# Performance work log

Measured on AMD Instinct MI355X. Metric: run time of the kernel, lower is better.

Reference implementation:

```python
import jax, jax.numpy as jnp
import numpy as np
from jax import lax


def _ln(x, g, b, eps=1e-5):
    m = jnp.mean(x, axis=-1, keepdims=True)
    v = jnp.mean((x - m) ** 2, axis=-1, keepdims=True)
    return (x - m) / jnp.sqrt(v + eps) * g + b


def _lin(x, w, b):  # torch Linear: w [out,in]
    return x @ w.T + b


def _conv(x, w, b, stride, pad):
    y = lax.conv_general_dilated(x, w, (stride, stride), pad,
                                 dimension_numbers=('NCHW', 'OIHW', 'NCHW'))
    return y + b[None, :, None, None]


def _haar_dwt(x):
    # J=1 haar, zero mode, even H/W: per 2x2 block [[a,b],[c,d]]
    a = x[:, :, 0::2, 0::2]
    bb = x[:, :, 0::2, 1::2]
    c = x[:, :, 1::2, 0::2]
    d = x[:, :, 1::2, 1::2]
    ll = (a + bb + c + d) * 0.5
    lohi = (a - bb + c - d) * 0.5  # band 0 (col-high)
    hilo = (a + bb - c - d) * 0.5  # band 1 (row-high)
    hihi = (a - bb - c + d) * 0.5  # band 2
    return ll, lohi, hilo, hihi


def _cross_attention(q, k, v):
    # q,k,v: [b, d, c]; 8 equal chunks along d; softmax over QUERY axis (torch dim=1)
    b, d, c = q.shape
    chunk = d // 8
    qc = q.reshape(b, 8, chunk, c)
    kc = k.reshape(b, 8, chunk, c)
    vc = v.reshape(b, 8, chunk, c)
    att = jnp.einsum('bnqc,bnkc->bnqk', qc, kc) * (8.0 ** -0.5)
    att = jax.nn.softmax(att, axis=2)  # normalize over q (matches F.softmax dim=1)
    out = jnp.einsum('bnqk,bnkc->bnqc', att, vc)
    return out.reshape(b, d, c)


def _ffn(x, ln1_g, ln1_b, fc1_w, fc1_b, div_w, div_b, fc2_w, fc2_b,
         ln3_g, ln3_b, fc3a_w, fc3a_b, fc3b_w, fc3b_b, lnn_g, lnn_b, act_w, act_b):
    x1 = jax.nn.gelu(_lin(_ln(x, ln1_g, ln1_b), fc1_w, fc1_b), approximate=False)
    x2 = jax.nn.gelu(_lin(x, div_w, div_b), approximate=False) - x1
    x2 = jax.nn.gelu(_lin(x2, fc2_w, fc2_b), approximate=False)
    x3 = _lin(jax.nn.gelu(_lin(_ln(x, ln3_g, ln3_b), fc3a_w, fc3a_b), approximate=False), fc3b_w, fc3b_b)
    gate = jax.nn.sigmoid(_lin(x, act_w, act_b))
    # dropout(0.5) is identity in eval mode
    return gate * _ln(x2 + x3, lnn_g, lnn_b)


def _resize_bilinear_ac(x, oh, ow):
    # bilinear, align_corners=True
    B, C, H, W = x.shape
    def idx(n_in, n_out):
        pos = jnp.linspace(0.0, n_in - 1.0, n_out)
        i0 = jnp.floor(pos).astype(jnp.int32)
        i1 = jnp.minimum(i0 + 1, n_in - 1)
        return i0, i1, (pos - i0).astype(x.dtype)
    y0, y1, wy = idx(H, oh)
    x0, x1, wx = idx(W, ow)
    r = x[:, :, y0, :] * (1 - wy)[None, None, :, None] + x[:, :, y1, :] * wy[None, None, :, None]
    return r[:, :, :, x0] * (1 - wx)[None, None, None, :] + r[:, :, :, x1] * wx[None, None, None, :]


def setup_inputs() -> dict:
    key = jax.random.key(0)
    ks = jax.random.split(key, 25)
    B, Cin, H, W = 16, 128, 128, 128
    Ch = 128  # out_planes // 2
    def nrm(k, shp, s=0.02):
        return jax.random.normal(k, shp, jnp.float32) * s
    inp = {
        'x': jax.random.normal(ks[0], (B, Cin, H, W), jnp.float32),
        'conv1_w': nrm(ks[1], (Ch, 2 * Cin, 1, 1)), 'conv1_b': jnp.zeros((Ch,), jnp.float32),
        'l1_w': nrm(ks[2], (Ch, Cin, 4, 4)), 'l1_b': jnp.zeros((Ch,), jnp.float32),
        'ln1_g': jnp.ones((Ch,), jnp.float32), 'ln1_b': jnp.zeros((Ch,), jnp.float32),
        'fc1_w': nrm(ks[3], (Ch, Ch)), 'fc1_b': jnp.zeros((Ch,), jnp.float32),
        'div_w': nrm(ks[4], (Ch, Ch)), 'div_b': jnp.zeros((Ch,), jnp.float32),
        'fc2_w': nrm(ks[5], (Ch, Ch)), 'fc2_b': jnp.zeros((Ch,), jnp.float32),
        'ln3_g': jnp.ones((Ch,), jnp.float32), 'ln3_b': jnp.zeros((Ch,), jnp.float32),
        'fc3a_w': nrm(ks[6], (Ch, Ch)), 'fc3a_b': jnp.zeros((Ch,), jnp.float32),
        'fc3b_w': nrm(ks[7], (Ch, Ch)), 'fc3b_b': jnp.zeros((Ch,), jnp.float32),
        'lnn_g': jnp.ones((Ch,), jnp.float32), 'lnn_b': jnp.zeros((Ch,), jnp.float32),
        'act_w': nrm(ks[8], (Ch, Ch)), 'act_b': jnp.zeros((Ch,), jnp.float32),
    }
    return inp


def reference(x, conv1_w, conv1_b, l1_w, l1_b, ln1_g, ln1_b, fc1_w, fc1_b,
              div_w, div_b, fc2_w, fc2_b, ln3_g, ln3_b, fc3a_w, fc3a_b,
              fc3b_w, fc3b_b, lnn_g, lnn_b, act_w, act_b):
    dw = jax.nn.relu(_conv(x, l1_w, l1_b, 2, ((1, 1), (1, 1))))
    yL, y_HL, y_LH, y_HH = _haar_dwt(x)
    y = _conv(jnp.concatenate((y_HL, y_LH), axis=1), conv1_w, conv1_b, 1, ((0, 0), (0, 0)))
    b, c, h, w = y.shape
    y_t = y.transpose(0, 2, 3, 1).reshape(b, h * w, c)
    yL_t = yL.transpose(0, 2, 3, 1).reshape(b, h * w, c)
    yHH_t = y_HH.transpose(0, 2, 3, 1).reshape(b, h * w, c)
    att = _cross_attention(yL_t, y_t, yHH_t)
    att = _ffn(att, ln1_g, ln1_b, fc1_w, fc1_b, div_w, div_b, fc2_w, fc2_b,
               ln3_g, ln3_b, fc3a_w, fc3a_b, fc3b_w, fc3b_b, lnn_g, lnn_b, act_w, act_b)
    att = att.reshape(b, h, w, c).transpose(0, 3, 1, 2)
    y_img = y_t.reshape(b, h, w, c).transpose(0, 3, 1, 2)
    down_2x = _resize_bilinear_ac(x, h, w)
    att = att * (down_2x - dw)
    return att + y_img
```

## Files before the change

kernel.cpp:

```cpp
#include <hip/hip_runtime.h>
#include <cmath>


#define EPI_NONE 0
#define EPI_EXP 5

typedef unsigned short u16;
typedef __bf16 v8bf __attribute__((ext_vector_type(8)));
typedef float f32x4 __attribute__((ext_vector_type(4)));

__device__ __forceinline__ float gelu_f(float v) {
  return 0.5f * v * (1.f + erff(v * 0.70710678118654752f));
}
__device__ __forceinline__ float sigmoid_f(float v) {
  return 1.f / (1.f + __expf(-v));
}
__device__ __forceinline__ float bf2f(u16 h) {
  return __uint_as_float((unsigned)h << 16);
}
__device__ __forceinline__ u16 f2bf(float f) {
  unsigned u = __float_as_uint(f);
  return (u16)((u + 0x7fffu + ((u >> 16) & 1u)) >> 16);
}
__device__ __forceinline__ unsigned f2bf_pk(float lo, float hi) {
  unsigned a = __float_as_uint(lo), b = __float_as_uint(hi);
  a = (a + 0x7fffu + ((a >> 16) & 1u)) >> 16;
  b = (b + 0x7fffu + ((b >> 16) & 1u)) >> 16;
  return a | (b << 16);
}
__device__ __forceinline__ void gld_lds16(const void* g, void* l) {
  __builtin_amdgcn_global_load_lds(
      (const __attribute__((address_space(1))) unsigned int*)g,
      (__attribute__((address_space(3))) unsigned int*)l, 16, 0, 0);
}

__global__ __launch_bounds__(256) void pre_k(const float* __restrict__ x,
                                             u16* __restrict__ yL16,
                                             u16* __restrict__ yHHt16,
                                             u16* __restrict__ hllh16,
                                             u16* __restrict__ xpt) {
  int gx = blockIdx.x;
  int jt = gx & 1, cit = gx >> 1;
  int i = blockIdx.y, b = blockIdx.z;
  int j0 = jt * 32, ci0 = cit * 32;
  int tx = threadIdx.x & 31, ty = threadIdx.x >> 5;
  __shared__ float sll[32][33], shl[32][33], slh[32][33], shh[32][33];
  if (gx == 0) {
    int pl = 1 + ((threadIdx.x >> 7) << 1);
    long off = ((long)(b * 4 + pl) * 4160 + (long)i * 65) * 128 + (threadIdx.x & 127);
    xpt[off] = 0;
  } else if (gx == 1) {
    int pl = (threadIdx.x >> 7) << 1;
    long off = ((long)(b * 4 + pl) * 4160 + (long)i * 65 + 64) * 128 + (threadIdx.x & 127);
    xpt[off] = 0;
  }
  const float2* x2 = (const float2*)x;
#pragma unroll
  for (int k = 0; k < 4; ++k) {
    int ci = ty + 8 * k;
    long base = (((long)b * 128 + ci0 + ci) * 128 + 2 * i) * 64 + j0 + tx;
    float2 ab = x2[base];
    float2 cd = x2[base + 64];
    float a = ab.x, bb = ab.y, c = cd.x, d = cd.y;
    sll[ci][tx] = (a + bb + c + d) * 0.5f;
    shl[ci][tx] = (a - bb + c - d) * 0.5f;
    slh[ci][tx] = (a + bb - c - d) * 0.5f;
    shh[ci][tx] = (a - bb - c + d) * 0.5f;
  }
  __syncthreads();
  long tok = (long)b * 4096 + i * 64 + j0;
  int r = threadIdx.x >> 3;
  int q4 = (threadIdx.x & 7) << 2;
  float vll[4], vhl[4], vlh[4], vhh[4];
#pragma unroll
  for (int e = 0; e < 4; ++e) {
    vll[e] = sll[q4 + e][r];
    vhl[e] = shl[q4 + e][r];
    vlh[e] = slh[q4 + e][r];
    vhh[e] = shh[q4 + e][r];
  }
  uint2 u;
  u.x = f2bf_pk(vll[0], vll[1]);
  u.y = f2bf_pk(vll[2], vll[3]);
  *(uint2*)(yL16 + (tok + r) * 128 + ci0 + q4) = u;
  u.x = f2bf_pk(vhl[0], vhl[1]);
  u.y = f2bf_pk(vhl[2], vhl[3]);
  *(uint2*)(hllh16 + (tok + r) * 256 + ci0 + q4) = u;
  u.x = f2bf_pk(vlh[0], vlh[1]);
  u.y = f2bf_pk(vlh[2], vlh[3]);
  *(uint2*)(hllh16 + (tok + r) * 256 + 128 + ci0 + q4) = u;
  {
    int ch = threadIdx.x >> 3;
    int t4 = (threadIdx.x & 7) << 2;
    uint2 h;
    h.x = f2bf_pk(shh[ch][t4], shh[ch][t4 + 1]);
    h.y = f2bf_pk(shh[ch][t4 + 2], shh[ch][t4 + 3]);
    *(uint2*)(yHHt16 + (long)(ci0 + ch) * 65536 + tok + t4) = h;
  }
  {
    long rb = (long)(b * 4) * 4160 + (long)i * 65;
    int ci = j0 + r;
    float pA[4], pB[4], pC[4], pD[4];
#pragma unroll
    for (int e = 0; e < 4; ++e) {
      pA[e] = 0.5f * (vll[e] + vhl[e] + vlh[e] + vhh[e]);
      pB[e] = 0.5f * (vll[e] - vhl[e] + vlh[e] - vhh[e]);
      pC[e] = 0.5f * (vll[e] + vhl[e] - vlh[e] - vhh[e]);
      pD[e] = 0.5f * (vll[e] - vhl[e] - vlh[e] + vhh[e]);
    }
    u.x = f2bf_pk(pA[0], pA[1]);
    u.y = f2bf_pk(pA[2], pA[3]);
    *(uint2*)(xpt + (rb + ci) * 128 + ci0 + q4) = u;
    u.x = f2bf_pk(pB[0], pB[1]);
    u.y = f2bf_pk(pB[2], pB[3]);
    *(uint2*)(xpt + (rb + 4160 + ci + 1) * 128 + ci0 + q4) = u;
    u.x = f2bf_pk(pC[0], pC[1]);
    u.y = f2bf_pk(pC[2], pC[3]);
    *(uint2*)(xpt + (rb + 8320 + ci) * 128 + ci0 + q4) = u;
    u.x = f2bf_pk(pD[0], pD[1]);
    u.y = f2bf_pk(pD[2], pD[3]);
    *(uint2*)(xpt + (rb + 12480 + ci + 1) * 128 + ci0 + q4) = u;
  }
}

__global__ __launch_bounds__(256) void wcvt8_k(
    const float* __restrict__ a0, const float* __restrict__ a1,
    const float* __restrict__ a2, const float* __restrict__ a3,
    const float* __restrict__ a4, const float* __restrict__ a5,
    const float* __restrict__ a6, const float* __restrict__ a7,
    unsigned* __restrict__ dst, unsigned* __restrict__ zp) {
  if (blockIdx.x >= 768) {
    zp[(blockIdx.x - 768) * 256 + threadIdx.x] = 0;
    return;
  }
  int f = blockIdx.x * 256 + threadIdx.x;
  int e = 2 * f;
  if (e < 262144) {
    int ch = e >> 13, kg = (e >> 10) & 7, n = (e >> 3) & 127, ke = e & 7;
    int k = ch * 64 + kg * 8 + ke;
    int stg = ch >> 2, sub = ch & 3;
    int kwsel = sub >> 1, chalf = sub & 1;
    int kh = stg >> 1, cp = stg & 1;
    int kw = cp ? (kwsel ? 2 : 0) : (kwsel ? 3 : 1);
    int c = chalf * 64 + (k & 63);
    long si = (((long)n * 128 + c) * 4 + kh) * 4 + kw;
    dst[f] = f2bf_pk(a0[si], a0[si + 16]);
    return;
  }
  const float* s; int b;
  if (e < 294912)      { s = a1; b = 262144; }
  else if (e < 311296) { s = a2; b = 294912; }
  else if (e < 327680) { s = a3; b = 311296; }
  else if (e < 344064) { s = a4; b = 327680; }
  else if (e < 360448) { s = a5; b = 344064; }
  else if (e < 376832) { s = a6; b = 360448; }
  else                 { s = a7; b = 376832; }
  dst[f] = f2bf_pk(s[e - b], s[e - b + 1]);
}

template <int AMODE, int EPI>
__global__ __launch_bounds__(256) void gemm16_k(
    const u16* __restrict__ A, long sA, int lda,
    const u16* __restrict__ B, long sB, int ldb,
    u16* __restrict__ C, long sC, int ldc,
    int K, float alpha, const float* __restrict__ bias,
    const u16* __restrict__ aux, const float* __restrict__ sc) {
  __shared__ __align__(16) char smem[32768];
  char* As = smem;
  char* Bs = smem + 16384;
  int z = blockIdx.z;
  int tid = threadIdx.x, lane = tid & 63, w = tid >> 6;
  int wm = w >> 1, wn = w & 1, l15 = lane & 15, l4 = lane >> 4;
  const u16* Ab = A + (long)z * sA + (long)blockIdx.x * 128 * lda;
  const u16* Bb = B + (long)z * sB + (long)blockIdx.y * 128 * ldb;
  const float* scz = (AMODE == 1) ? sc + (long)z * K : nullptr;
  int sm = tid >> 3, skg = tid & 7;
  int sbase = sm * 128 + ((skg ^ (sm & 7)) << 4);
  uint4 pa[4], pb[4];

  auto loadAB = [&](int k0) {
#pragma unroll
    for (int u = 0; u < 4; ++u) {
      pb[u] = *(const uint4*)(Bb + (long)(sm + 32 * u) * ldb + k0 + skg * 8);
      uint4 v = *(const uint4*)(Ab + (long)(sm + 32 * u) * lda + k0 + skg * 8);
      if (AMODE == 1) {
        float4 s0 = *(const float4*)(scz + k0 + skg * 8);
        float4 s1 = *(const float4*)(scz + k0 + skg * 8 + 4);
        v.x = f2bf_pk(bf2f((u16)(v.x & 0xffff)) * s0.x, bf2f((u16)(v.x >> 16)) * s0.y);
        v.y = f2bf_pk(bf2f((u16)(v.y & 0xffff)) * s0.z, bf2f((u16)(v.y >> 16)) * s0.w);
        v.z = f2bf_pk(bf2f((u16)(v.z & 0xffff)) * s1.x, bf2f((u16)(v.z >> 16)) * s1.y);
        v.w = f2bf_pk(bf2f((u16)(v.w & 0xffff)) * s1.z, bf2f((u16)(v.w >> 16)) * s1.w);
      }
      pa[u] = v;
    }
  };

  f32x4 acc[4][4] = {};
  loadAB(0);
  int nch = K >> 6;
  for (int ch = 0; ch < nch; ++ch) {
    __syncthreads();
#pragma unroll
    for (int u = 0; u < 4; ++u) {
      *(uint4*)(As + sbase + u * 4096) = pa[u];
      *(uint4*)(Bs + sbase + u * 4096) = pb[u];
    }
    __syncthreads();
    if (ch + 1 < nch) loadAB((ch + 1) << 6);
#pragma unroll
    for (int s = 0; s < 2; ++s) {
      int ko = (((s << 2) | l4) ^ (l15 & 7)) << 4;
      v8bf af[4], bfr[4];
#pragma unroll
      for (int t = 0; t < 4; ++t) {
        af[t] = *(const v8bf*)(As + (64 * wm + 16 * t + l15) * 128 + ko);
        bfr[t] = *(const v8bf*)(Bs + (64 * wn + 16 * t + l15) * 128 + ko);
      }
#pragma unroll
      for (int mt = 0; mt < 4; ++mt)
#pragma unroll
        for (int nt = 0; nt < 4; ++nt)
          acc[mt][nt] = __builtin_amdgcn_mfma_f32_16x16x32_bf16(af[mt], bfr[nt], acc[mt][nt], 0, 0, 0);
    }
  }
  u16* Cb = C + (long)z * sC;
#pragma unroll
  for (int mt = 0; mt < 4; ++mt) {
#pragma unroll
    for (int nt = 0; nt < 4; ++nt) {
      f32x4 a = acc[mt][nt];
      int n = blockIdx.y * 128 + 64 * wn + 16 * nt + l15;
      float bv = bias ? bias[n] : 0.f;
#pragma unroll
      for (int r = 0; r < 4; ++r) {
        long m = (long)blockIdx.x * 128 + 64 * wm + 16 * mt + 4 * l4 + r;
        float v = a[r] * alpha + bv;
        if (EPI == EPI_EXP) v = __expf(v);
        Cb[m * ldc + n] = f2bf(v);
      }
    }
  }
}

__global__ __launch_bounds__(256) void ffn_k(
    const u16* __restrict__ Xg,
    const u16* __restrict__ w_fc1, const u16* __restrict__ w_div,
    const u16* __restrict__ w_fc2, const u16* __restrict__ w_fc3a,
    const u16* __restrict__ w_fc3b, const u16* __restrict__ w_act,
    const float* __restrict__ b_fc1, const float* __restrict__ b_div,
    const float* __restrict__ b_fc2, const float* __restrict__ b_fc3a,
    const float* __restrict__ b_fc3b, const float* __restrict__ b_act,
    const float* __restrict__ ln1g, const float* __restrict__ ln1b,
    const float* __restrict__ ln3g, const float* __restrict__ ln3b,
    const float* __restrict__ lnng, const float* __restrict__ lnnb,
    u16* __restrict__ out) {
  __shared__ __align__(16) char smem[49152];
  char* X = smem;
  char* A = smem + 16384;
  char* E = smem + 32768;
  int z = blockIdx.x;
  long t0 = (long)z * 64;
  int tid = threadIdx.x, lane = tid & 63, w = tid >> 6;
  int wm = w >> 1, wn = w & 1, l15 = lane & 15, l4 = lane >> 4;

  {
    const u16* src = Xg + t0 * 128;
#pragma unroll
    for (int r = 0; r < 4; ++r) {
      int u = r * 256 + tid;
      int row = u >> 4, cg = u & 15;
      gld_lds16(src + row * 128 + ((cg ^ (row & 7)) << 3),
                X + (r * 256 + w * 64) * 16);
    }
  }

  auto gemm = [&](const char* Asrc, const u16* Bg, f32x4 (&acc)[2][4]) {
#pragma unroll
    for (int mt = 0; mt < 2; ++mt)
#pragma unroll
      for (int nt = 0; nt < 4; ++nt) acc[mt][nt] = f32x4{0.f, 0.f, 0.f, 0.f};
#pragma unroll
    for (int s = 0; s < 4; ++s) {
      v8bf af[2], bw[4];
#pragma unroll
      for (int mt = 0; mt < 2; ++mt) {
        int row = 32 * wm + 16 * mt + l15;
        af[mt] = *(const v8bf*)(Asrc + row * 256 + (((s * 4 + l4) ^ (row & 7)) << 4));
      }
#pragma unroll
      for (int nt = 0; nt < 4; ++nt) {
        int rn = 64 * wn + 16 * nt + l15;
        bw[nt] = *(const v8bf*)(Bg + rn * 128 + (s * 4 + l4) * 8);
      }
#pragma unroll
      for (int mt = 0; mt < 2; ++mt)
#pragma unroll
        for (int nt = 0; nt < 4; ++nt)
          acc[mt][nt] = __builtin_amdgcn_mfma_f32_16x16x32_bf16(
              af[mt], bw[nt], acc[mt][nt], 0, 0, 0);
    }
  };

  auto epi = [&](f32x4 (&acc)[2][4], const float* bias, char* dst,
                 const char* Eb, int mode) {
#pragma unroll
    for (int nt = 0; nt < 4; ++nt) {
      int n = 64 * wn + 16 * nt + l15;
      float bv = bias[n];
#pragma unroll
      for (int mt = 0; mt < 2; ++mt) {
#pragma unroll
        for (int r = 0; r < 4; ++r) {
          int m = 32 * wm + 16 * mt + 4 * l4 + r;
          int off = m * 256 + (((n >> 3) ^ (m & 7)) << 4) + (n & 7) * 2;
          float v = acc[mt][nt][r] + bv;
          if (mode == 0) v = gelu_f(v);
          else if (mode == 1) v = gelu_f(v) - bf2f(*(const u16*)(Eb + off));
          else if (mode == 2) v += bf2f(*(const u16*)(Eb + off));
          else v = sigmoid_f(v);
          *(u16*)(dst + off) = f2bf(v);
        }
      }
    }
  };

  auto lnpass = [&](const char* src, char* dst, const float* g,
                    const float* bt) {
    int row = w * 16 + (lane >> 2), q = lane & 3;
    float v[32];
    float s = 0.f, sq = 0.f;
#pragma unroll
    for (int gi = 0; gi < 4; ++gi) {
      int gr = q * 4 + gi;
      v8bf hv = *(const v8bf*)(src + row * 256 + ((gr ^ (row & 7)) << 4));
#pragma unroll
      for (int e = 0; e < 8; ++e) {
        float f = bf2f(((const u16*)&hv)[e]);
        v[gi * 8 + e] = f;
        s += f;
        sq += f * f;
      }
    }
    s += __shfl_xor(s, 1); sq += __shfl_xor(sq, 1);
    s += __shfl_xor(s, 2); sq += __shfl_xor(sq, 2);
    float mean = s * 0.0078125f;
    float rstd = rsqrtf(sq * 0.0078125f - mean * mean + 1e-5f);
#pragma unroll
    for (int gi = 0; gi < 4; ++gi) {
      int gr = q * 4 + gi;
      int c0 = gr * 8;
      unsigned o[4];
#pragma unroll
      for (int e = 0; e < 4; ++e) {
        float y0 = (v[gi * 8 + 2 * e] - mean) * rstd * g[c0 + 2 * e] + bt[c0 + 2 * e];
        float y1 = (v[gi * 8 + 2 * e + 1] - mean) * rstd * g[c0 + 2 * e + 1] + bt[c0 + 2 * e + 1];
        o[e] = f2bf_pk(y0, y1);
      }
      *(uint4*)(dst + row * 256 + ((gr ^ (row & 7)) << 4)) = *(uint4*)o;
    }
  };

  f32x4 acc[2][4];
  __syncthreads();
  lnpass(X, A, ln1g, ln1b); __syncthreads();
  gemm(A, w_fc1, acc); __syncthreads();
  epi(acc, b_fc1, E, nullptr, 0); __syncthreads();
  gemm(X, w_div, acc); __syncthreads();
  epi(acc, b_div, A, E, 1); __syncthreads();
  gemm(A, w_fc2, acc); __syncthreads();
  epi(acc, b_fc2, E, nullptr, 0); __syncthreads();
  lnpass(X, A, ln3g, ln3b); __syncthreads();
  gemm(A, w_fc3a, acc); __syncthreads();
  epi(acc, b_fc3a, A, nullptr, 0); __syncthreads();
  gemm(A, w_fc3b, acc); __syncthreads();
  epi(acc, b_fc3b, A, E, 2); __syncthreads();
  gemm(X, w_act, acc); __syncthreads();
  epi(acc, b_act, E, nullptr, 3); __syncthreads();

  {
    int row = w * 16 + (lane >> 2), q = lane & 3;
    float v[32];
    float s = 0.f, sq = 0.f;
#pragma unroll
    for (int gi = 0; gi < 4; ++gi) {
      int gr = q * 4 + gi;
      v8bf hv = *(const v8bf*)(A + row * 256 + ((gr ^ (row & 7)) << 4));
#pragma unroll
      for (int e = 0; e < 8; ++e) {
        float f = bf2f(((const u16*)&hv)[e]);
        v[gi * 8 + e] = f;
        s += f;
        sq += f * f;
      }
    }
    s += __shfl_xor(s, 1); sq += __shfl_xor(sq, 1);
    s += __shfl_xor(s, 2); sq += __shfl_xor(sq, 2);
    float mean = s * 0.0078125f;
    float rstd = rsqrtf(sq * 0.0078125f - mean * mean + 1e-5f);
    u16* og = out + (t0 + row) * 128;
#pragma unroll
    for (int gi = 0; gi < 4; ++gi) {
      int gr = q * 4 + gi;
      int c0 = gr * 8;
      v8bf gv = *(const v8bf*)(E + row * 256 + ((gr ^ (row & 7)) << 4));
      unsigned o[4];
#pragma unroll
      for (int e = 0; e < 4; ++e) {
        float y0 = ((v[gi * 8 + 2 * e] - mean) * rstd * lnng[c0 + 2 * e] + lnnb[c0 + 2 * e]) *
                   bf2f(((const u16*)&gv)[2 * e]);
        float y1 = ((v[gi * 8 + 2 * e + 1] - mean) * rstd * lnng[c0 + 2 * e + 1] + lnnb[c0 + 2 * e + 1]) *
                   bf2f(((const u16*)&gv)[2 * e + 1]);
        o[e] = f2bf_pk(y0, y1);
      }
      *(uint4*)(og + c0) = *(uint4*)o;
    }
  }
}

__global__ __launch_bounds__(256) __attribute__((amdgpu_waves_per_eu(4)))
void conv4g_k(const u16* __restrict__ xpt, const u16* __restrict__ wb,
              const float* __restrict__ bias, const u16* __restrict__ zp,
              u16* __restrict__ dw16) {
  __shared__ __align__(16) char smem[33280];
  char* As = smem;
  int raw = blockIdx.x;
  int swz = (raw & 7) * 128 + (raw >> 3);
  int oi = swz & 63, b = swz >> 6;
  int tid = threadIdx.x, lane = tid & 63, w = tid >> 6;
  int wm = w >> 1, wn = w & 1, l15 = lane & 15, l4 = lane >> 4;
  f32x4 acc[2][4] = {};

  auto issueA = [&](int stg2, int bsel) {
    int kh = stg2 >> 1, cp2 = stg2 & 1;
    int roff = (kh == 0) ? -1 : (kh == 3) ? 1 : 0;
    int ri = oi + roff;
    int ph = (((kh + 1) & 1) << 1) | cp2;
    const u16* rowb = ((unsigned)ri < 64u)
        ? xpt + ((long)(b * 4 + ph) * 4160 + (long)ri * 65) * 128
        : zp;
    char* lb = As + bsel * 16640 + w * 1024;
#pragma unroll
    for (int i = 0; i < 4; ++i) {
      int d = i * 4096 + w * 1024 + lane * 16;
      int slot = d >> 8, cg = (d >> 4) & 15;
      gld_lds16(rowb + slot * 128 + ((cg ^ ((slot - cp2) & 7)) << 3),
                lb + i * 4096);
    }
    if (tid < 16) {
      gld_lds16(rowb + 64 * 128 + ((lane ^ ((64 - cp2) & 7)) << 3),
                As + bsel * 16640 + 16384);
    }
  };

  issueA(0, 0);
  for (int stg = 0; stg < 8; ++stg) {
    __syncthreads();
    if (stg < 7) issueA(stg + 1, (stg + 1) & 1);
    const char* Ab = As + (stg & 1) * 16640;
    int cp2 = stg & 1;
#pragma unroll
    for (int sub = 0; sub < 4; ++sub) {
      int chunk = stg * 4 + sub;
      const int kwsel = sub >> 1, chalf = sub & 1;
#pragma unroll
      for (int s = 0; s < 2; ++s) {
        v8bf bw[4], af[2];
#pragma unroll
        for (int nt = 0; nt < 4; ++nt) {
          int row = 64 * wn + 16 * nt + l15;
          bw[nt] = *(const v8bf*)(wb + ((long)(chunk * 8 + s * 4 + l4) * 128 + row) * 8);
        }
#pragma unroll
        for (int mt = 0; mt < 2; ++mt) {
          int slot = 32 * wm + 16 * mt + l15 + kwsel;
          int cg = chalf * 8 + s * 4 + l4;
          af[mt] = *(const v8bf*)(Ab + slot * 256 + ((cg ^ ((slot - cp2) & 7)) << 4));
        }
#pragma unroll
        for (int mt = 0; mt < 2; ++mt)
#pragma unroll
          for (int nt = 0; nt < 4; ++nt)
            acc[mt][nt] = __builtin_amdgcn_mfma_f32_16x16x32_bf16(
                af[mt], bw[nt], acc[mt][nt], 0, 0, 0);
      }
    }
  }
  __syncthreads();
  float* buf = (float*)(smem + w * 2176);
  long obase = ((long)b * 128) * 4096 + oi * 64;
#pragma unroll
  for (int cg = 0; cg < 4; ++cg) {
    int co = 64 * wn + 16 * cg + l15;
    float bv = bias[co];
#pragma unroll
    for (int mt = 0; mt < 2; ++mt) {
      f32x4 a = acc[mt][cg];
#pragma unroll
      for (int r = 0; r < 4; ++r)
        buf[l15 * 34 + 16 * mt + 4 * l4 + r] = fmaxf(a[r] + bv, 0.f);
    }
    __syncthreads();
#pragma unroll
    for (int it = 0; it < 8; ++it) {
      int row = it * 2 + (lane >> 5);
      int mcol = lane & 31;
      int coz = 64 * wn + 16 * cg + row;
      dw16[obase + (long)coz * 4096 + 32 * wm + mcol] = f2bf(buf[row * 34 + mcol]);
    }
    __syncthreads();
  }
}

__global__ __launch_bounds__(256) void ssum_k(const u16* __restrict__ E,
                                              float* __restrict__ sc) {
  int z = blockIdx.y;
  int k = blockIdx.x * 256 + threadIdx.x;
  const u16* Eb = E + (long)z * 262144 + k;
  float s = 0.f;
#pragma unroll 8
  for (int q = 0; q < 512; ++q) s += bf2f(Eb[(long)q * 512]);
  sc[(long)z * 512 + k] = 1.f / s;
}

__global__ __launch_bounds__(256) void combine_k(const u16* __restrict__ attf,
                                                 const u16* __restrict__ yt,
                                                 const u16* __restrict__ dw16,
                                                 const float* __restrict__ x,
                                                 float* __restrict__ out) {
  int gx = blockIdx.x;
  int jt = gx & 1, cot = gx >> 1;
  int i = blockIdx.y, b = blockIdx.z;
  int j0 = jt * 32, co0 = cot * 32;
  int tx = threadIdx.x & 31, ty = threadIdx.x >> 5;
  __shared__ float sa[32][33], sy[32][33];
  long tokbase = (long)b * 4096 + i * 64 + j0;
#pragma unroll
  for (int k = 0; k < 4; ++k) {
    int row = ty + 8 * k;
    long idx = (tokbase + row) * 128 + co0 + tx;
    sa[row][tx] = bf2f(attf[idx]);
    sy[row][tx] = bf2f(yt[idx]);
  }
  __syncthreads();
  float py = (float)(i * 127) / 63.0f;
  int y0 = (int)py;
  int y1 = min(y0 + 1, 127);
  float wy = py - (float)y0;
  int j = j0 + tx;
  float px = (float)(j * 127) / 63.0f;
  int x0 = (int)px;
  int x1 = min(x0 + 1, 127);
  float wx = px - (float)x0;
#pragma unroll
  for (int k = 0; k < 4; ++k) {
    int co = co0 + ty + 8 * k;
    const float* xb = x + (((long)b * 128 + co) * 128) * 128;
    float r0 = xb[y0 * 128 + x0] * (1.f - wx) + xb[y0 * 128 + x1] * wx;
    float r1 = xb[y1 * 128 + x0] * (1.f - wx) + xb[y1 * 128 + x1] * wx;
    float d2 = r0 * (1.f - wy) + r1 * wy;
    long oidx = (((long)b * 128 + co) * 64 + i) * 64 + j;
    float dwv = bf2f(dw16[oidx]);
    out[oidx] = sa[tx][ty + 8 * k] * (d2 - dwv) + sy[tx][ty + 8 * k];
  }
}

extern "C" void kernel_launch(void* const* d_in, const int* in_sizes, int n_in,
                              void* d_out, int out_size, void* d_ws, size_t ws_size,
                              hipStream_t stream) {
  const float* x = (const float*)d_in[0];
  const float* w1 = (const float*)d_in[1];
  const float* b1 = (const float*)d_in[2];
  const float* l1w = (const float*)d_in[3];
  const float* l1b = (const float*)d_in[4];
  const float* ln1g = (const float*)d_in[5];
  const float* ln1b = (const float*)d_in[6];
  const float* fc1w = (const float*)d_in[7];
  const float* fc1b = (const float*)d_in[8];
  const float* divw = (const float*)d_in[9];
  const float* divb = (const float*)d_in[10];
  const float* fc2w = (const float*)d_in[11];
  const float* fc2b = (const float*)d_in[12];
  const float* ln3g = (const float*)d_in[13];
  const float* ln3b = (const float*)d_in[14];
  const float* fc3aw = (const float*)d_in[15];
  const float* fc3ab = (const float*)d_in[16];
  const float* fc3bw = (const float*)d_in[17];
  const float* fc3bb = (const float*)d_in[18];
  const float* lnng = (const float*)d_in[19];
  const float* lnnb = (const float*)d_in[20];
  const float* actw = (const float*)d_in[21];
  const float* actb = (const float*)d_in[22];

  char* W = (char*)d_ws;
  u16* yL16 = (u16*)(W);
  u16* hllh16 = (u16*)(W + 16777216L);
  u16* yHHt16 = (u16*)(W + 50331648L);
  u16* y16 = (u16*)(W + 67108864L);
  u16* S16 = (u16*)(W + 83886080L);
  u16* attO16 = (u16*)(W + 150994944L);
  u16* dw16 = (u16*)(W + 167772160L);
  u16* t2 = (u16*)(W + 201326592L);
  float* sc = (float*)(W + 251658240L);
  u16* wall = (u16*)(W + 251920384L);
  u16* l1wb = wall;
  u16* w1b = wall + 262144;
  u16* fc1b16 = wall + 294912;
  u16* divb16 = wall + 311296;
  u16* fc2b16 = wall + 327680;
  u16* fc3ab16 = wall + 344064;
  u16* fc3bb16 = wall + 360448;
  u16* actb16 = wall + 376832;
  u16* xpt16 = S16;
  u16* zp16 = (u16*)(W + 152043520L);

  dim3 blk(256);
  const float qk_scale = 0.35355339059327373f;

  wcvt8_k<<<dim3(785), blk, 0, stream>>>(l1w, w1, fc1w, divw, fc2w, fc3aw,
                                         fc3bw, actw, (unsigned*)wall,
                                         (unsigned*)zp16);
  pre_k<<<dim3(8, 64, 16), blk, 0, stream>>>(x, yL16, yHHt16, hllh16, xpt16);
  gemm16_k<0, EPI_NONE><<<dim3(512, 1, 1), blk, 0, stream>>>(
      hllh16, 0, 256, w1b, 0, 256, y16, 0, 128, 256, 1.f, b1, nullptr, nullptr);
  conv4g_k<<<dim3(1024), blk, 0, stream>>>(xpt16, l1wb, l1b, zp16, dw16);
  gemm16_k<0, EPI_EXP><<<dim3(4, 4, 128), blk, 0, stream>>>(
      yL16, 65536, 128, y16, 65536, 128, S16, 262144, 512, 128, qk_scale,
      nullptr, nullptr, nullptr);
  ssum_k<<<dim3(2, 128), blk, 0, stream>>>(S16, sc);
  gemm16_k<1, EPI_NONE><<<dim3(4, 1, 128), blk, 0, stream>>>(
      S16, 262144, 512, yHHt16, 512, 65536, attO16, 65536, 128, 512, 1.f,
      nullptr, nullptr, sc);
  ffn_k<<<dim3(1024), blk, 0, stream>>>(
      attO16, fc1b16, divb16, fc2b16, fc3ab16, fc3bb16, actb16,
      fc1b, divb, fc2b, fc3ab, fc3bb, actb,
      ln1g, ln1b, ln3g, ln3b, lnng, lnnb, t2);
  combine_k<<<dim3(8, 64, 16), blk, 0, stream>>>(t2, y16, dw16, x, (float*)d_out);
}
```

Baseline: 610.0 us.

## Keep FFN intermediates in registers to shrink LDS and raise occupancy

The fused FFN kernel now holds the GELU and sigmoid intermediates in packed bf16 registers rather than a third 16 KB LDS buffer. This cuts shared memory from 48 KB to 32 KB and adds a waves-per-EU hint so more blocks can be resident per CU. The GEMM order is rearranged so the gate GEMM runs before fc3b, which drops several barriers, and the gate is written into the X buffer at the end. The cost is higher register pressure, which could cause spills under the occupancy hint.

Result: slower. 841.5 us (+38.0%).

```diff
diff --git a/kernel.cpp b/kernel.cpp
--- a/kernel.cpp
+++ b/kernel.cpp
@@ -242,7 +242,8 @@
   }
 }
 
-__global__ __launch_bounds__(256) void ffn_k(
+__global__ __launch_bounds__(256) __attribute__((amdgpu_waves_per_eu(4)))
+void ffn_k(
     const u16* __restrict__ Xg,
     const u16* __restrict__ w_fc1, const u16* __restrict__ w_div,
     const u16* __restrict__ w_fc2, const u16* __restrict__ w_fc3a,
@@ -254,10 +255,9 @@
     const float* __restrict__ ln3g, const float* __restrict__ ln3b,
     const float* __restrict__ lnng, const float* __restrict__ lnnb,
     u16* __restrict__ out) {
-  __shared__ __align__(16) char smem[49152];
+  __shared__ __align__(16) char smem[32768];
   char* X = smem;
   char* A = smem + 16384;
-  char* E = smem + 32768;
   int z = blockIdx.x;
   long t0 = (long)z * 64;
   int tid = threadIdx.x, lane = tid & 63, w = tid >> 6;
@@ -301,8 +301,27 @@
     }
   };
 
-  auto epi = [&](f32x4 (&acc)[2][4], const float* bias, char* dst,
-                 const char* Eb, int mode) {
+  auto epi_reg = [&](f32x4 (&acc)[2][4], const float* bias,
+                     unsigned (&er)[16], int mode) {
+#pragma unroll
+    for (int nt = 0; nt < 4; ++nt) {
+      float bv = bias[64 * wn + 16 * nt + l15];
+#pragma unroll
+      for (int mt = 0; mt < 2; ++mt) {
+#pragma unroll
+        for (int rp = 0; rp < 2; ++rp) {
+          float v0 = acc[mt][nt][2 * rp] + bv;
+          float v1 = acc[mt][nt][2 * rp + 1] + bv;
+          if (mode == 0) { v0 = gelu_f(v0); v1 = gelu_f(v1); }
+          else           { v0 = sigmoid_f(v0); v1 = sigmoid_f(v1); }
+          er[nt * 4 + mt * 2 + rp] = f2bf_pk(v0, v1);
+        }
+      }
+    }
+  };
+
+  auto epi_lds = [&](f32x4 (&acc)[2][4], const float* bias, char* dst,
+                     const unsigned (&er)[16], int mode) {
 #pragma unroll
     for (int nt = 0; nt < 4; ++nt) {
       int n = 64 * wn + 16 * nt + l15;
@@ -313,12 +332,29 @@
         for (int r = 0; r < 4; ++r) {
           int m = 32 * wm + 16 * mt + 4 * l4 + r;
           int off = m * 256 + (((n >> 3) ^ (m & 7)) << 4) + (n & 7) * 2;
+          float ev = bf2f((u16)(er[nt * 4 + mt * 2 + (r >> 1)] >> (16 * (r & 1))));
           float v = acc[mt][nt][r] + bv;
-          if (mode == 0) v = gelu_f(v);
-          else if (mode == 1) v = gelu_f(v) - bf2f(*(const u16*)(Eb + off));
-          else if (mode == 2) v += bf2f(*(const u16*)(Eb + off));
-          else v = sigmoid_f(v);
+          if (mode == 0) v = gelu_f(v) - ev;
+          else if (mode == 1) v = gelu_f(v);
+          else v += ev;
           *(u16*)(dst + off) = f2bf(v);
+        }
+      }
+    }
+  };
+
+  auto reg_to_lds = [&](const unsigned (&er)[16], char* dst) {
+#pragma unroll
+    for (int nt = 0; nt < 4; ++nt) {
+      int n = 64 * wn + 16 * nt + l15;
+#pragma unroll
+      for (int mt = 0; mt < 2; ++mt) {
+#pragma unroll
+        for (int r = 0; r < 4; ++r) {
+          int m = 32 * wm + 16 * mt + 4 * l4 + r;
+          int off = m * 256 + (((n >> 3) ^ (m & 7)) << 4) + (n & 7) * 2;
+          *(u16*)(dst + off) =
+              (u16)(er[nt * 4 + mt * 2 + (r >> 1)] >> (16 * (r & 1)));
         }
       }
     }
@@ -361,21 +397,32 @@
   };
 
   f32x4 acc[2][4];
-  __syncthreads();
-  lnpass(X, A, ln1g, ln1b); __syncthreads();
-  gemm(A, w_fc1, acc); __syncthreads();
-  epi(acc, b_fc1, E, nullptr, 0); __syncthreads();
-  gemm(X, w_div, acc); __syncthreads();
-  epi(acc, b_div, A, E, 1); __syncthreads();
-  gemm(A, w_fc2, acc); __syncthreads();
-  epi(acc, b_fc2, E, nullptr, 0); __syncthreads();
-  lnpass(X, A, ln3g, ln3b); __syncthreads();
-  gemm(A, w_fc3a, acc); __syncthreads();
-  epi(acc, b_fc3a, A, nullptr, 0); __syncthreads();
-  gemm(A, w_fc3b, acc); __syncthreads();
-  epi(acc, b_fc3b, A, E, 2); __syncthreads();
-  gemm(X, w_act, acc); __syncthreads();
-  epi(acc, b_act, E, nullptr, 3); __syncthreads();
+  unsigned e1[16], e2[16], sg[16];
+  __syncthreads();
+  lnpass(X, A, ln1g, ln1b);
+  __syncthreads();
+  gemm(A, w_fc1, acc);
+  epi_reg(acc, b_fc1, e1, 0);
+  gemm(X, w_div, acc);
+  __syncthreads();
+  epi_lds(acc, b_div, A, e1, 0);
+  __syncthreads();
+  gemm(A, w_fc2, acc);
+  epi_reg(acc, b_fc2, e2, 0);
+  __syncthreads();
+  lnpass(X, A, ln3g, ln3b);
+  __syncthreads();
+  gemm(A, w_fc3a, acc);
+  __syncthreads();
+  epi_lds(acc, b_fc3a, A, e1, 1);
+  __syncthreads();
+  gemm(X, w_act, acc);
+  epi_reg(acc, b_act, sg, 1);
+  gemm(A, w_fc3b, acc);
+  __syncthreads();
+  epi_lds(acc, b_fc3b, A, e2, 2);
+  reg_to_lds(sg, X);
+  __syncthreads();
 
   {
     int row = w * 16 + (lane >> 2), q = lane & 3;
@@ -402,7 +449,7 @@
     for (int gi = 0; gi < 4; ++gi) {
       int gr = q * 4 + gi;
       int c0 = gr * 8;
-      v8bf gv = *(const v8bf*)(E + row * 256 + ((gr ^ (row & 7)) << 4));
+      v8bf gv = *(const v8bf*)(X + row * 256 + ((gr ^ (row & 7)) << 4));
       unsigned o[4];
 #pragma unroll
       for (int e = 0; e < 4; ++e) {
```
